# Kernel optimization log

Measured on AMD Instinct MI355X. Metric: run time of the kernel, lower is better.

## Reference

```python
import jax, jax.numpy as jnp
import numpy as np

N = 10000      # nodes
E = 160000     # edges (avg degree 16)
H = 128        # hidden_dim
L = 4          # propagation_depth
G = 64         # graphs in batch
ATOM_V = 119
BOND_V = 5
AVG_D_LOG = 1.0
EPS_SCALE = 1e-8


def setup_inputs() -> dict:
    key = jax.random.key(0)
    ks = jax.random.split(key, 12)
    x = jax.random.randint(ks[0], (N,), 0, ATOM_V)
    edge_index = jax.random.randint(ks[1], (2, E), 0, N)
    edge_attr = jax.random.randint(ks[2], (E,), 0, BOND_V)
    batch = jnp.sort(jax.random.randint(ks[3], (N,), 0, G))
    atom_emb = jax.random.normal(ks[4], (ATOM_V, H), jnp.float32) * 0.1
    bond_emb = jax.random.normal(ks[5], (BOND_V, H), jnp.float32) * 0.1
    pre_W = jax.random.normal(ks[6], (L, 3 * H, H), jnp.float32) / np.sqrt(3 * H)
    pre_b = jnp.zeros((L, H), jnp.float32)
    post_W = jax.random.normal(ks[7], (L, 10 * H, H), jnp.float32) / np.sqrt(10 * H)
    post_b = jnp.zeros((L, H), jnp.float32)
    out_W1 = jax.random.normal(ks[8], (3 * H, H), jnp.float32) / np.sqrt(3 * H)
    out_b1 = jnp.zeros((H,), jnp.float32)
    out_W2 = jax.random.normal(ks[9], (H, 1), jnp.float32) / np.sqrt(H)
    out_b2 = jnp.zeros((1,), jnp.float32)
    return {"x": x, "edge_index": edge_index, "edge_attr": edge_attr, "batch": batch,
            "atom_emb": atom_emb, "bond_emb": bond_emb,
            "pre_W": pre_W, "pre_b": pre_b, "post_W": post_W, "post_b": post_b,
            "out_W1": out_W1, "out_b1": out_b1, "out_W2": out_W2, "out_b2": out_b2}


def _seg_mean_sum_max(v, idx, num_seg, cnt):
    s = jax.ops.segment_sum(v, idx, num_segments=num_seg)
    mean = s / jnp.maximum(cnt, 1.0)[:, None]
    mx = jax.ops.segment_max(v, idx, num_segments=num_seg)
    mx = jnp.where(cnt[:, None] > 0, mx, 0.0)  # empty segments -> 0 (torch scatter)
    return mean, s, mx


def _clean(a):
    return jnp.where(jnp.isnan(a) | jnp.isinf(a), 0.0, a)


def reference(x, edge_index, edge_attr, batch, atom_emb, bond_emb,
              pre_W, pre_b, post_W, post_b, out_W1, out_b1, out_W2, out_b2):
    h = atom_emb[x]            # [N, H] atom encoder
    e = bond_emb[edge_attr]    # [E, H] bond encoder
    row, col = edge_index[0], edge_index[1]
    n = h.shape[0]
    deg = jax.ops.segment_sum(jnp.ones_like(col, jnp.float32), col, num_segments=n)
    D = deg[:, None]
    logD = jnp.log(D + 1.0)
    amp_fac = logD / AVG_D_LOG                       # amplification scaler
    att_fac = AVG_D_LOG / jnp.maximum(logD, EPS_SCALE)  # attenuation scaler
    n_layers = pre_W.shape[0]
    for l in range(n_layers):
        h_in = h
        z2 = jnp.concatenate([h[row], h[col], e], axis=-1)         # [E, 3H]
        msg = z2 @ pre_W[l] + pre_b[l]                             # pretrans (1 layer, no act)
        mean, s, mx = _seg_mean_sum_max(msg, col, n, deg)
        hagg = jnp.concatenate([mean, s, mx], axis=-1)             # [N, 3H]
        hcat = jnp.concatenate([hagg, hagg * amp_fac, hagg * att_fac, h_in], axis=-1)  # [N, 10H]
        h = hcat @ post_W[l] + post_b[l]                           # posttrans (1 layer)
        h = h + h_in                                               # residual
    # readout over graphs
    cnt = jax.ops.segment_sum(jnp.ones((n,), jnp.float32), batch, num_segments=G)
    rmean, rsum, rmax = _seg_mean_sum_max(h, batch, G, cnt)
    r = _clean(jnp.concatenate([rmean, rsum, rmax], axis=-1))      # [G, 3H]
    out = jax.nn.relu(r @ out_W1 + out_b1) @ out_W2 + out_b2       # [G, 1]
    return _clean(out)
```

## Files before the change

kernel.cpp:

```cpp
#include <hip/hip_runtime.h>
#include <hip/hip_bf16.h>
#include <math.h>

#define NN 10000
#define NE 160000
#define HD 128
#define NL 4
#define NG 64

typedef __attribute__((ext_vector_type(8))) short bf16x8;
typedef __attribute__((ext_vector_type(4))) short bf16x4;
typedef __attribute__((ext_vector_type(4))) float f32x4;

static __device__ __forceinline__ short f2bf(float f) {
    unsigned u = __float_as_uint(f);
    unsigned r = (u + 0x7FFFu + ((u >> 16) & 1u)) >> 16;
    return (short)r;
}
static __device__ __forceinline__ float bf2f(short s) {
    return __uint_as_float(((unsigned)(unsigned short)s) << 16);
}

__global__ void setup1_kernel(const int* __restrict__ x, const float* __restrict__ atom_emb,
                              float* __restrict__ h, float* __restrict__ deg,
                              int* __restrict__ cursor) {
    int idx = blockIdx.x * 256 + threadIdx.x;
    if (idx < NN) { deg[idx] = 0.f; cursor[idx] = 0; }
    if (idx < NN * HD) {
        int n = idx >> 7, f = idx & 127;
        h[idx] = atom_emb[x[n] * HD + f];
    }
}

__global__ __launch_bounds__(256) void setup2_kernel(
    const int* __restrict__ col, float* __restrict__ deg,
    const float* __restrict__ bond_emb,
    const float* __restrict__ pre_W, const float* __restrict__ pre_b,
    const float* __restrict__ post_W,
    float* __restrict__ btab, short* __restrict__ pre_Wt, short* __restrict__ post_Wt) {
    int b = blockIdx.x;
    if (b < 625) {
        int e = b * 256 + threadIdx.x;
        if (e < NE) atomicAdd(&deg[col[e]], 1.f);
        return;
    }
    if (b < 645) {
        int lb = b - 625;
        if (threadIdx.x < 128) {
            int l = lb / 5, bb = lb % 5;
            int f = threadIdx.x;
            const float* W2 = pre_W + (size_t)l * 384 * HD + 256 * HD;
            const float* eb = bond_emb + bb * HD;
            float acc = pre_b[l * HD + f];
            for (int k = 0; k < HD; ++k) acc = fmaf(eb[k], W2[k * HD + f], acc);
            btab[(l * 5 + bb) * HD + f] = acc;
        }
        return;
    }
    int idx = (b - 645) * 256 + threadIdx.x;
    if (idx < NL * 4 * 256 * 32) {
        int l = idx >> 15;
        int r = idx & 32767;
        int kblk = r >> 13;
        int rr = r & 8191;
        int j = rr >> 5, k = rr & 31;
        const float* Wl = pre_W + (size_t)l * 384 * HD;
        float v = (j < 128) ? Wl[(kblk * 32 + k) * HD + j]
                            : Wl[(128 + kblk * 32 + k) * HD + (j - 128)];
        pre_Wt[idx] = f2bf(v);
    }
    if (idx < NL * 40 * 128 * 32) {
        int l = idx / 163840;
        int r = idx % 163840;
        int kblk = r >> 12;
        int rr = r & 4095;
        int j = rr >> 5, k = rr & 31;
        post_Wt[idx] = f2bf(post_W[(size_t)l * 163840 + (size_t)(kblk * 32 + k) * HD + j]);
    }
}

__global__ __launch_bounds__(1024) void scan_facs_kernel(const float* __restrict__ deg,
                                                         int* __restrict__ offsets,
                                                         float* __restrict__ amp,
                                                         float* __restrict__ att) {
    __shared__ int s[1024];
    int t = threadIdx.x;
    int base = t * 10;
    int v[10];
    int lsum = 0;
    #pragma unroll
    for (int i = 0; i < 10; ++i) {
        int idx = base + i;
        int d = (idx < NN) ? (int)deg[idx] : 0;
        v[i] = d;
        lsum += d;
        if (idx < NN) {
            float logD = logf((float)d + 1.f);
            amp[idx] = logD;
            att[idx] = 1.f / fmaxf(logD, 1e-8f);
        }
    }
    s[t] = lsum;
    __syncthreads();
    for (int off = 1; off < 1024; off <<= 1) {
        int x2 = (t >= off) ? s[t - off] : 0;
        __syncthreads();
        s[t] += x2;
        __syncthreads();
    }
    int run = s[t] - lsum;
    #pragma unroll
    for (int i = 0; i < 10; ++i) {
        int idx = base + i;
        if (idx < NN) offsets[idx] = run;
        run += v[i];
    }
    if (t == 1023) offsets[NN] = run;
}

__global__ void scatter_kernel(const int* __restrict__ row, const int* __restrict__ col,
                               const int* __restrict__ ea, const int* __restrict__ offsets,
                               int* __restrict__ cursor, int* __restrict__ perm) {
    int e = blockIdx.x * 256 + threadIdx.x;
    if (e < NE) {
        int c = col[e];
        int pos = offsets[c] + atomicAdd(&cursor[c], 1);
        perm[pos] = row[e] | (ea[e] << 14);
    }
}

__global__ __launch_bounds__(256) void pre_gemm_mfma(const float* __restrict__ h,
                                                     const short* __restrict__ Wt,
                                                     short* __restrict__ hw0,
                                                     float* __restrict__ hw1) {
    __shared__ short Ap[16][136];
    int t = threadIdx.x;
    int nb = blockIdx.x * 16;
    {
        int nl = t >> 4, f = (t & 15) * 8;
        int n = nb + nl;
        const float* src = h + (size_t)n * HD + f;
        float4 x0 = *(const float4*)src, x1 = *(const float4*)(src + 4);
        bf16x8 pk;
        pk[0]=f2bf(x0.x); pk[1]=f2bf(x0.y); pk[2]=f2bf(x0.z); pk[3]=f2bf(x0.w);
        pk[4]=f2bf(x1.x); pk[5]=f2bf(x1.y); pk[6]=f2bf(x1.z); pk[7]=f2bf(x1.w);
        *(bf16x8*)&Ap[nl][f] = pk;
    }
    __syncthreads();
    int wave = t >> 6, lane = t & 63;
    int lx = lane & 15, kb = lane >> 4;
    f32x4 acc[4];
    #pragma unroll
    for (int j = 0; j < 4; ++j) acc[j] = (f32x4){0.f, 0.f, 0.f, 0.f};

    for (int ks = 0; ks < 4; ++ks) {
        bf16x8 a = *(const bf16x8*)&Ap[lx][ks * 32 + kb * 8];
        const short* bp = Wt + (size_t)ks * 8192 + (size_t)(wave * 64 + lx) * 32 + kb * 8;
        #pragma unroll
        for (int jj = 0; jj < 4; ++jj) {
            bf16x8 bfr = *(const bf16x8*)(bp + jj * 512);
            acc[jj] = __builtin_amdgcn_mfma_f32_16x16x32_bf16(a, bfr, acc[jj], 0, 0, 0);
        }
    }
    #pragma unroll
    for (int jj = 0; jj < 4; ++jj) {
        int c = wave * 64 + jj * 16 + lx;
        #pragma unroll
        for (int r_ = 0; r_ < 4; ++r_) {
            int n2 = nb + kb * 4 + r_;
            if (c < 128) hw0[(size_t)n2 * HD + c] = f2bf(acc[jj][r_]);
            else         hw1[(size_t)n2 * HD + (c - 128)] = acc[jj][r_];
        }
    }
}

__global__ __launch_bounds__(256) void agg_node_gemm_mfma(
    const short* __restrict__ hw0, const float* __restrict__ hw1,
    const float* __restrict__ btab,
    const int* __restrict__ offsets, const int* __restrict__ perm,
    const float* __restrict__ hin,
    const float* __restrict__ amp, const float* __restrict__ att,
    const short* __restrict__ Wt , const float* __restrict__ bias,
    float* __restrict__ hout,
    const short* __restrict__ nextWt ,
    short* __restrict__ hw0n, float* __restrict__ hw1n) {
    __shared__ short Ap[16][1288];
    __shared__ short Ap2[16][136];
    __shared__ float btab_s[5][128];
    int t = threadIdx.x;
    int nb = blockIdx.x * 16;

    if (t < 160) {
        int b = t >> 5, f4 = (t & 31) * 4;
        *(f32x4*)&btab_s[b][f4] = *(const f32x4*)(btab + b * HD + f4);
    }
    __syncthreads();

    {
        int nl = t >> 4;
        int n = nb + nl;
        int f = (t & 15) * 8;
        int s0 = offsets[n];
        int d = offsets[n + 1] - s0;
        f32x4 sum0 = {0.f,0.f,0.f,0.f}, sum1 = {0.f,0.f,0.f,0.f};
        f32x4 mx0 = {-INFINITY,-INFINITY,-INFINITY,-INFINITY};
        f32x4 mx1 = mx0;
        int i = 0;
        for (; i + 2 <= d; i += 2) {
            int p0 = perm[s0 + i], p1 = perm[s0 + i + 1];
            bf16x8 a0 = *(const bf16x8*)(hw0 + (size_t)(p0 & 16383) * HD + f);
            bf16x8 a1 = *(const bf16x8*)(hw0 + (size_t)(p1 & 16383) * HD + f);
            const float* t0 = &btab_s[p0 >> 14][f];
            const float* t1 = &btab_s[p1 >> 14][f];
            f32x4 b00 = *(const f32x4*)t0, b01 = *(const f32x4*)(t0 + 4);
            f32x4 b10 = *(const f32x4*)t1, b11 = *(const f32x4*)(t1 + 4);
            f32x4 v00, v01, v10, v11;
            #pragma unroll
            for (int q = 0; q < 4; ++q) {
                v00[q] = bf2f(a0[q]) + b00[q];
                v01[q] = bf2f(a0[q + 4]) + b01[q];
                v10[q] = bf2f(a1[q]) + b10[q];
                v11[q] = bf2f(a1[q + 4]) + b11[q];
            }
            sum0 += v00 + v10; sum1 += v01 + v11;
            #pragma unroll
            for (int q = 0; q < 4; ++q) {
                mx0[q] = fmaxf(mx0[q], fmaxf(v00[q], v10[q]));
                mx1[q] = fmaxf(mx1[q], fmaxf(v01[q], v11[q]));
            }
        }
        if (i < d) {
            int p0 = perm[s0 + i];
            bf16x8 a0 = *(const bf16x8*)(hw0 + (size_t)(p0 & 16383) * HD + f);
            const float* t0 = &btab_s[p0 >> 14][f];
            f32x4 b00 = *(const f32x4*)t0, b01 = *(const f32x4*)(t0 + 4);
            f32x4 v00, v01;
            #pragma unroll
            for (int q = 0; q < 4; ++q) {
                v00[q] = bf2f(a0[q]) + b00[q];
                v01[q] = bf2f(a0[q + 4]) + b01[q];
            }
            sum0 += v00; sum1 += v01;
            #pragma unroll
            for (int q = 0; q < 4; ++q) {
                mx0[q] = fmaxf(mx0[q], v00[q]);
                mx1[q] = fmaxf(mx1[q], v01[q]);
            }
        }
        const float* cp = hw1 + (size_t)n * HD + f;
        f32x4 c0 = *(const f32x4*)cp, c1 = *(const f32x4*)(cp + 4);
        f32x4 me0, me1, so0, so1, mo0, mo1;
        if (d > 0) {
            float df = (float)d, di = 1.f / df;
            so0 = sum0 + df * c0;  so1 = sum1 + df * c1;
            me0 = sum0 * di + c0;  me1 = sum1 * di + c1;
            mo0 = mx0 + c0;        mo1 = mx1 + c1;
        } else {
            me0 = (f32x4){0.f,0.f,0.f,0.f}; me1 = me0;
            so0 = me0; so1 = me0; mo0 = me0; mo1 = me0;
        }
        float f_amp = amp[n], f_att = att[n];
        #pragma unroll
        for (int fi = 0; fi < 3; ++fi) {
            float fac = (fi == 0) ? 1.f : ((fi == 1) ? f_amp : f_att);
            #pragma unroll
            for (int ag = 0; ag < 3; ++ag) {
                f32x4 r0 = (ag == 0) ? me0 : ((ag == 1) ? so0 : mo0);
                f32x4 r1 = (ag == 0) ? me1 : ((ag == 1) ? so1 : mo1);
                bf16x8 pk;
                #pragma unroll
                for (int q = 0; q < 4; ++q) {
                    pk[q]     = f2bf(r0[q] * fac);
                    pk[q + 4] = f2bf(r1[q] * fac);
                }
                *(bf16x8*)&Ap[nl][(fi * 3 + ag) * 128 + f] = pk;
            }
        }
        {
            const float* src = hin + (size_t)n * HD + f;
            float4 x0 = *(const float4*)src, x1 = *(const float4*)(src + 4);
            bf16x8 pk;
            pk[0]=f2bf(x0.x); pk[1]=f2bf(x0.y); pk[2]=f2bf(x0.z); pk[3]=f2bf(x0.w);
            pk[4]=f2bf(x1.x); pk[5]=f2bf(x1.y); pk[6]=f2bf(x1.z); pk[7]=f2bf(x1.w);
            *(bf16x8*)&Ap[nl][9 * 128 + f] = pk;
        }
    }
    __syncthreads();

    int wave = t >> 6, lane = t & 63;
    int lx = lane & 15, kb = lane >> 4;
    f32x4 acc0 = {0.f,0.f,0.f,0.f}, acc1 = acc0;
    for (int ks = 0; ks < 40; ++ks) {
        bf16x8 a = *(const bf16x8*)&Ap[lx][ks * 32 + kb * 8];
        const short* bp = Wt + (size_t)ks * 4096 + (size_t)(wave * 32 + lx) * 32 + kb * 8;
        bf16x8 b0 = *(const bf16x8*)bp;
        bf16x8 b1 = *(const bf16x8*)(bp + 512);
        acc0 = __builtin_amdgcn_mfma_f32_16x16x32_bf16(a, b0, acc0, 0, 0, 0);
        acc1 = __builtin_amdgcn_mfma_f32_16x16x32_bf16(a, b1, acc1, 0, 0, 0);
    }
    #pragma unroll
    for (int jj = 0; jj < 2; ++jj) {
        int c = wave * 32 + jj * 16 + lx;
        float bc = bias[c];
        f32x4 av = jj ? acc1 : acc0;
        #pragma unroll
        for (int r_ = 0; r_ < 4; ++r_) {
            int n2 = nb + kb * 4 + r_;
            size_t off = (size_t)n2 * HD + c;
            float ho = av[r_] + bc + hin[off];
            hout[off] = ho;
            Ap2[n2 - nb][c] = f2bf(ho);
        }
    }
    if (nextWt == nullptr) return;
    __syncthreads();

    f32x4 acc[4];
    #pragma unroll
    for (int j = 0; j < 4; ++j) acc[j] = (f32x4){0.f, 0.f, 0.f, 0.f};
    for (int ks = 0; ks < 4; ++ks) {
        bf16x8 a = *(const bf16x8*)&Ap2[lx][ks * 32 + kb * 8];
        const short* bp = nextWt + (size_t)ks * 8192 + (size_t)(wave * 64 + lx) * 32 + kb * 8;
        #pragma unroll
        for (int jj = 0; jj < 4; ++jj) {
            bf16x8 bfr = *(const bf16x8*)(bp + jj * 512);
            acc[jj] = __builtin_amdgcn_mfma_f32_16x16x32_bf16(a, bfr, acc[jj], 0, 0, 0);
        }
    }
    #pragma unroll
    for (int jj = 0; jj < 4; ++jj) {
        int c = wave * 64 + jj * 16 + lx;
        #pragma unroll
        for (int r_ = 0; r_ < 4; ++r_) {
            int n2 = nb + kb * 4 + r_;
            if (c < 128) hw0n[(size_t)n2 * HD + c] = f2bf(acc[jj][r_]);
            else         hw1n[(size_t)n2 * HD + (c - 128)] = acc[jj][r_];
        }
    }
}

__global__ __launch_bounds__(256) void pool_out_kernel(
    const float* __restrict__ h, const int* __restrict__ batch,
    const float* __restrict__ W1, const float* __restrict__ b1,
    const float* __restrict__ W2, const float* __restrict__ b2,
    float* __restrict__ out)
{
    __shared__ float rs[384];
    __shared__ float red[256];
    __shared__ float s2[128], m2[128];
    int g = blockIdx.x, t = threadIdx.x;
    int lo = 0, hi = NN;
    while (lo < hi) { int mid = (lo + hi) >> 1; if (batch[mid] < g) lo = mid + 1; else hi = mid; }
    int lo2 = lo, hi2 = NN;
    while (lo2 < hi2) { int mid = (lo2 + hi2) >> 1; if (batch[mid] < g + 1) lo2 = mid + 1; else hi2 = mid; }
    int cnt = lo2 - lo;
    int f = t & 127, grp = t >> 7;
    float sum = 0.f, mx = -INFINITY;
    for (int n = lo + grp; n < lo2; n += 2) {
        float v = h[(size_t)n * HD + f];
        sum += v; mx = fmaxf(mx, v);
    }
    if (grp == 1) { s2[f] = sum; m2[f] = mx; }
    __syncthreads();
    if (grp == 0) {
        sum += s2[f]; mx = fmaxf(mx, m2[f]);
        float mean = (cnt > 0) ? sum / (float)cnt : 0.f;
        float so = (cnt > 0) ? sum : 0.f;
        float mo = (cnt > 0) ? mx : 0.f;
        if (isnan(mean) || isinf(mean)) mean = 0.f;
        if (isnan(so) || isinf(so)) so = 0.f;
        if (isnan(mo) || isinf(mo)) mo = 0.f;
        rs[f] = mean; rs[128 + f] = so; rs[256 + f] = mo;
    }
    __syncthreads();
    {
        int j = t & 127, kh = t >> 7;
        float acc = 0.f;
        for (int k = kh * 192; k < kh * 192 + 192; ++k)
            acc = fmaf(rs[k], W1[k * HD + j], acc);
        red[t] = acc;
    }
    __syncthreads();
    if (t < 128) {
        float v = fmaxf(red[t] + red[128 + t] + b1[t], 0.f);
        red[t] = v * W2[t];
    }
    __syncthreads();
    for (int s = 64; s > 0; s >>= 1) {
        if (t < s) red[t] += red[t + s];
        __syncthreads();
    }
    if (t == 0) {
        float o = red[0] + b2[0];
        if (isnan(o) || isinf(o)) o = 0.f;
        out[g] = o;
    }
}

extern "C" void kernel_launch(void* const* d_in, const int* in_sizes, int n_in,
                              void* d_out, int out_size, void* d_ws, size_t ws_size,
                              hipStream_t stream)
{
    const int* x          = (const int*)d_in[0];
    const int* ei         = (const int*)d_in[1];
    const int* ea         = (const int*)d_in[2];
    const int* batch      = (const int*)d_in[3];
    const float* atom_emb = (const float*)d_in[4];
    const float* bond_emb = (const float*)d_in[5];
    const float* pre_W    = (const float*)d_in[6];
    const float* pre_b    = (const float*)d_in[7];
    const float* post_W   = (const float*)d_in[8];
    const float* post_b   = (const float*)d_in[9];
    const float* out_W1   = (const float*)d_in[10];
    const float* out_b1   = (const float*)d_in[11];
    const float* out_W2   = (const float*)d_in[12];
    const float* out_b2   = (const float*)d_in[13];
    float* out = (float*)d_out;
    const int* row = ei;
    const int* col = ei + NE;

    char* p = (char*)d_ws;
    auto alloc = [&](size_t bytes) { char* r = p; p += (bytes + 255) & ~(size_t)255; return r; };
    float*    deg     = (float*)alloc((size_t)NN * 4);
    float*    amp     = (float*)alloc((size_t)NN * 4);
    float*    att     = (float*)alloc((size_t)NN * 4);
    int*      offsets = (int*)alloc((size_t)(NN + 1) * 4);
    int*      cursor  = (int*)alloc((size_t)NN * 4);
    int*      perm    = (int*)alloc((size_t)NE * 4);
    float*    hA      = (float*)alloc((size_t)NN * HD * 4);
    float*    hB      = (float*)alloc((size_t)NN * HD * 4);
    short*    hw0A    = (short*)alloc((size_t)NN * HD * 2);
    short*    hw0B    = (short*)alloc((size_t)NN * HD * 2);
    float*    hw1A    = (float*)alloc((size_t)NN * HD * 4);
    float*    hw1B    = (float*)alloc((size_t)NN * HD * 4);
    float*    btab    = (float*)alloc((size_t)NL * 5 * HD * 4);
    short*    pre_Wt  = (short*)alloc((size_t)NL * 4 * 256 * 32 * 2);
    short*    post_Wt = (short*)alloc((size_t)NL * 40 * 128 * 32 * 2);

    setup1_kernel<<<(NN * HD) / 256, 256, 0, stream>>>(x, atom_emb, hA, deg, cursor);
    setup2_kernel<<<645 + (NL * 40 * 128 * 32 + 255) / 256, 256, 0, stream>>>(
        col, deg, bond_emb, pre_W, pre_b, post_W, btab, pre_Wt, post_Wt);
    scan_facs_kernel<<<1, 1024, 0, stream>>>(deg, offsets, amp, att);
    scatter_kernel<<<(NE + 255) / 256, 256, 0, stream>>>(row, col, ea, offsets, cursor, perm);

    pre_gemm_mfma<<<NN / 16, 256, 0, stream>>>(hA, pre_Wt, hw0A, hw1A);

    float* curH = hA;
    float* nxtH = hB;
    for (int l = 0; l < NL; ++l) {
        short* hw0_in  = (l & 1) ? hw0B : hw0A;
        float* hw1_in  = (l & 1) ? hw1B : hw1A;
        short* hw0_out = (l & 1) ? hw0A : hw0B;
        float* hw1_out = (l & 1) ? hw1A : hw1B;
        const short* nextWt = (l + 1 < NL) ? (pre_Wt + (size_t)(l + 1) * 4 * 256 * 32) : nullptr;
        agg_node_gemm_mfma<<<NN / 16, 256, 0, stream>>>(
            hw0_in, hw1_in, btab + (size_t)l * 5 * HD, offsets, perm,
            curH, amp, att, post_Wt + (size_t)l * 40 * 128 * 32,
            post_b + (size_t)l * HD, nxtH, nextWt, hw0_out, hw1_out);
        float* tmp = curH; curH = nxtH; nxtH = tmp;
    }

    pool_out_kernel<<<NG, 256, 0, stream>>>(curH, batch, out_W1, out_b1, out_W2, out_b2, out);
}
```

Baseline: 287.5 us.

## Shrink fused layer LDS by storing only base aggregates and scaling in GEMM

The fused aggregation plus post-transform kernel now keeps only the mean, sum and max aggregates in shared memory, about 19.5 KB instead of roughly 44 KB. The amp and att scaled copies are rebuilt on the fly inside the MFMA loop, and the residual input h is read from global memory and converted per k-step. The edge gather is unrolled to four neighbours per iteration, and launch bounds request 4 blocks per SM. The aim is higher occupancy and more memory-level parallelism in the gather, at the cost of extra bf16 convert and multiply work plus global loads inside the GEMM loop, and an extra bf16 rounding of the scaled terms.

```diff
diff --git a/kernel.cpp b/kernel.cpp
--- a/kernel.cpp
+++ b/kernel.cpp
@@ -7,6 +7,8 @@
 #define HD 128
 #define NL 4
 #define NG 64
+#define NBLK 625
+#define SMEM_BYTES 19584
 
 typedef __attribute__((ext_vector_type(8))) short bf16x8;
 typedef __attribute__((ext_vector_type(4))) short bf16x4;
@@ -129,10 +131,10 @@
     }
 }
 
-__global__ __launch_bounds__(256) void pre_gemm_mfma(const float* __restrict__ h,
-                                                     const short* __restrict__ Wt,
-                                                     short* __restrict__ hw0,
-                                                     float* __restrict__ hw1) {
+__global__ __launch_bounds__(256, 4) void pre_gemm_kernel(const float* __restrict__ h,
+                                                          const short* __restrict__ Wt,
+                                                          short* __restrict__ hw0,
+                                                          float* __restrict__ hw1) {
     __shared__ short Ap[16][136];
     int t = threadIdx.x;
     int nb = blockIdx.x * 16;
@@ -152,7 +154,7 @@
     f32x4 acc[4];
     #pragma unroll
     for (int j = 0; j < 4; ++j) acc[j] = (f32x4){0.f, 0.f, 0.f, 0.f};
-
+    #pragma unroll
     for (int ks = 0; ks < 4; ++ks) {
         bf16x8 a = *(const bf16x8*)&Ap[lx][ks * 32 + kb * 8];
         const short* bp = Wt + (size_t)ks * 8192 + (size_t)(wave * 64 + lx) * 32 + kb * 8;
@@ -174,25 +176,25 @@
     }
 }
 
-__global__ __launch_bounds__(256) void agg_node_gemm_mfma(
-    const short* __restrict__ hw0, const float* __restrict__ hw1,
-    const float* __restrict__ btab,
+__global__ __launch_bounds__(256, 4) void fused_kernel(
+    const short* __restrict__ hw0_in, const float* __restrict__ hw1_in,
+    const float* __restrict__ btabL,
     const int* __restrict__ offsets, const int* __restrict__ perm,
-    const float* __restrict__ hin,
+    const float* __restrict__ curH,
     const float* __restrict__ amp, const float* __restrict__ att,
     const short* __restrict__ Wt , const float* __restrict__ bias,
-    float* __restrict__ hout,
-    const short* __restrict__ nextWt ,
-    short* __restrict__ hw0n, float* __restrict__ hw1n) {
-    __shared__ short Ap[16][1288];
-    __shared__ short Ap2[16][136];
-    __shared__ float btab_s[5][128];
+    float* __restrict__ nxtH,
+    const short* __restrict__ nextWt, short* __restrict__ hw0o, float* __restrict__ hw1o) {
+    __shared__ __align__(16) char smem[SMEM_BYTES];
+    short (*aggB)[3][132] = (short(*)[3][132])smem;
+    float (*btab_s)[128]  = (float(*)[128])(smem + 12672);
+    short (*Ap2)[136]     = (short(*)[136])(smem + 15232);
     int t = threadIdx.x;
     int nb = blockIdx.x * 16;
 
     if (t < 160) {
-        int b = t >> 5, f4 = (t & 31) * 4;
-        *(f32x4*)&btab_s[b][f4] = *(const f32x4*)(btab + b * HD + f4);
+        int bb = t >> 5, f4 = (t & 31) * 4;
+        *(f32x4*)&btab_s[bb][f4] = *(const f32x4*)(btabL + bb * HD + f4);
     }
     __syncthreads();
 
@@ -206,48 +208,47 @@
         f32x4 mx0 = {-INFINITY,-INFINITY,-INFINITY,-INFINITY};
         f32x4 mx1 = mx0;
         int i = 0;
-        for (; i + 2 <= d; i += 2) {
-            int p0 = perm[s0 + i], p1 = perm[s0 + i + 1];
-            bf16x8 a0 = *(const bf16x8*)(hw0 + (size_t)(p0 & 16383) * HD + f);
-            bf16x8 a1 = *(const bf16x8*)(hw0 + (size_t)(p1 & 16383) * HD + f);
+        for (; i + 4 <= d; i += 4) {
+            int p0 = perm[s0 + i],     p1 = perm[s0 + i + 1];
+            int p2 = perm[s0 + i + 2], p3 = perm[s0 + i + 3];
+            bf16x8 a0 = *(const bf16x8*)(hw0_in + (size_t)(p0 & 16383) * HD + f);
+            bf16x8 a1 = *(const bf16x8*)(hw0_in + (size_t)(p1 & 16383) * HD + f);
+            bf16x8 a2 = *(const bf16x8*)(hw0_in + (size_t)(p2 & 16383) * HD + f);
+            bf16x8 a3 = *(const bf16x8*)(hw0_in + (size_t)(p3 & 16383) * HD + f);
             const float* t0 = &btab_s[p0 >> 14][f];
             const float* t1 = &btab_s[p1 >> 14][f];
-            f32x4 b00 = *(const f32x4*)t0, b01 = *(const f32x4*)(t0 + 4);
-            f32x4 b10 = *(const f32x4*)t1, b11 = *(const f32x4*)(t1 + 4);
-            f32x4 v00, v01, v10, v11;
+            const float* t2 = &btab_s[p2 >> 14][f];
+            const float* t3 = &btab_s[p3 >> 14][f];
             #pragma unroll
             for (int q = 0; q < 4; ++q) {
-                v00[q] = bf2f(a0[q]) + b00[q];
-                v01[q] = bf2f(a0[q + 4]) + b01[q];
-                v10[q] = bf2f(a1[q]) + b10[q];
-                v11[q] = bf2f(a1[q + 4]) + b11[q];
+                float v00 = bf2f(a0[q]) + t0[q];
+                float v01 = bf2f(a0[q+4]) + t0[q+4];
+                float v10 = bf2f(a1[q]) + t1[q];
+                float v11 = bf2f(a1[q+4]) + t1[q+4];
+                float v20 = bf2f(a2[q]) + t2[q];
+                float v21 = bf2f(a2[q+4]) + t2[q+4];
+                float v30 = bf2f(a3[q]) + t3[q];
+                float v31 = bf2f(a3[q+4]) + t3[q+4];
+                sum0[q] += (v00 + v10) + (v20 + v30);
+                sum1[q] += (v01 + v11) + (v21 + v31);
+                mx0[q] = fmaxf(fmaxf(fmaxf(mx0[q], v00), fmaxf(v10, v20)), v30);
+                mx1[q] = fmaxf(fmaxf(fmaxf(mx1[q], v01), fmaxf(v11, v21)), v31);
             }
-            sum0 += v00 + v10; sum1 += v01 + v11;
+        }
+        for (; i < d; ++i) {
+            int p0 = perm[s0 + i];
+            bf16x8 a0 = *(const bf16x8*)(hw0_in + (size_t)(p0 & 16383) * HD + f);
+            const float* t0 = &btab_s[p0 >> 14][f];
             #pragma unroll
             for (int q = 0; q < 4; ++q) {
-                mx0[q] = fmaxf(mx0[q], fmaxf(v00[q], v10[q]));
-                mx1[q] = fmaxf(mx1[q], fmaxf(v01[q], v11[q]));
+                float v00 = bf2f(a0[q]) + t0[q];
+                float v01 = bf2f(a0[q+4]) + t0[q+4];
+                sum0[q] += v00; sum1[q] += v01;
+                mx0[q] = fmaxf(mx0[q], v00);
+                mx1[q] = fmaxf(mx1[q], v01);
             }
         }
-        if (i < d) {
-            int p0 = perm[s0 + i];
-            bf16x8 a0 = *(const bf16x8*)(hw0 + (size_t)(p0 & 16383) * HD + f);
-            const float* t0 = &btab_s[p0 >> 14][f];
-            f32x4 b00 = *(const f32x4*)t0, b01 = *(const f32x4*)(t0 + 4);
-            f32x4 v00, v01;
-            #pragma unroll
-            for (int q = 0; q < 4; ++q) {
-                v00[q] = bf2f(a0[q]) + b00[q];
-                v01[q] = bf2f(a0[q + 4]) + b01[q];
-            }
-            sum0 += v00; sum1 += v01;
-            #pragma unroll
-            for (int q = 0; q < 4; ++q) {
-                mx0[q] = fmaxf(mx0[q], v00[q]);
-                mx1[q] = fmaxf(mx1[q], v01[q]);
-            }
-        }
-        const float* cp = hw1 + (size_t)n * HD + f;
+        const float* cp = hw1_in + (size_t)n * HD + f;
         f32x4 c0 = *(const f32x4*)cp, c1 = *(const f32x4*)(cp + 4);
         f32x4 me0, me1, so0, so1, mo0, mo1;
         if (d > 0) {
@@ -259,44 +260,52 @@
             me0 = (f32x4){0.f,0.f,0.f,0.f}; me1 = me0;
             so0 = me0; so1 = me0; mo0 = me0; mo1 = me0;
         }
-        float f_amp = amp[n], f_att = att[n];
-        #pragma unroll
-        for (int fi = 0; fi < 3; ++fi) {
-            float fac = (fi == 0) ? 1.f : ((fi == 1) ? f_amp : f_att);
-            #pragma unroll
-            for (int ag = 0; ag < 3; ++ag) {
-                f32x4 r0 = (ag == 0) ? me0 : ((ag == 1) ? so0 : mo0);
-                f32x4 r1 = (ag == 0) ? me1 : ((ag == 1) ? so1 : mo1);
-                bf16x8 pk;
-                #pragma unroll
-                for (int q = 0; q < 4; ++q) {
-                    pk[q]     = f2bf(r0[q] * fac);
-                    pk[q + 4] = f2bf(r1[q] * fac);
-                }
-                *(bf16x8*)&Ap[nl][(fi * 3 + ag) * 128 + f] = pk;
-            }
-        }
-        {
-            const float* src = hin + (size_t)n * HD + f;
-            float4 x0 = *(const float4*)src, x1 = *(const float4*)(src + 4);
-            bf16x8 pk;
-            pk[0]=f2bf(x0.x); pk[1]=f2bf(x0.y); pk[2]=f2bf(x0.z); pk[3]=f2bf(x0.w);
-            pk[4]=f2bf(x1.x); pk[5]=f2bf(x1.y); pk[6]=f2bf(x1.z); pk[7]=f2bf(x1.w);
-            *(bf16x8*)&Ap[nl][9 * 128 + f] = pk;
-        }
+        bf16x8 pk;
+        #pragma unroll
+        for (int q = 0; q < 4; ++q) { pk[q] = f2bf(me0[q]); pk[q+4] = f2bf(me1[q]); }
+        *(bf16x8*)&aggB[nl][0][f] = pk;
+        #pragma unroll
+        for (int q = 0; q < 4; ++q) { pk[q] = f2bf(so0[q]); pk[q+4] = f2bf(so1[q]); }
+        *(bf16x8*)&aggB[nl][1][f] = pk;
+        #pragma unroll
+        for (int q = 0; q < 4; ++q) { pk[q] = f2bf(mo0[q]); pk[q+4] = f2bf(mo1[q]); }
+        *(bf16x8*)&aggB[nl][2][f] = pk;
     }
     __syncthreads();
 
     int wave = t >> 6, lane = t & 63;
     int lx = lane & 15, kb = lane >> 4;
+    int n_lx = nb + lx;
+    float famp = amp[n_lx], fatt = att[n_lx];
+    const float* hsrc = curH + (size_t)n_lx * HD;
+    const short* bbase = Wt + (size_t)(wave * 32 + lx) * 32 + kb * 8;
     f32x4 acc0 = {0.f,0.f,0.f,0.f}, acc1 = acc0;
+    #pragma unroll
     for (int ks = 0; ks < 40; ++ks) {
-        bf16x8 a = *(const bf16x8*)&Ap[lx][ks * 32 + kb * 8];
-        const short* bp = Wt + (size_t)ks * 4096 + (size_t)(wave * 32 + lx) * 32 + kb * 8;
+        constexpr int KS4096 = 4096;
+        int r = ks >> 2;
+        int kk = (ks & 3) * 32 + kb * 8;
+        bf16x8 afrag;
+        if (r < 9) {
+            int ag = r % 3, fi = r / 3;
+            bf16x8 raw = *(const bf16x8*)&aggB[lx][ag][kk];
+            if (fi == 0) afrag = raw;
+            else {
+                float fac = (fi == 1) ? famp : fatt;
+                #pragma unroll
+                for (int q = 0; q < 8; ++q) afrag[q] = f2bf(bf2f(raw[q]) * fac);
+            }
+        } else {
+            const float* src = hsrc + kk;
+            float4 x0 = *(const float4*)src, x1 = *(const float4*)(src + 4);
+            afrag[0]=f2bf(x0.x); afrag[1]=f2bf(x0.y); afrag[2]=f2bf(x0.z); afrag[3]=f2bf(x0.w);
+            afrag[4]=f2bf(x1.x); afrag[5]=f2bf(x1.y); afrag[6]=f2bf(x1.z); afrag[7]=f2bf(x1.w);
+        }
+        const short* bp = bbase + (size_t)ks * KS4096;
         bf16x8 b0 = *(const bf16x8*)bp;
         bf16x8 b1 = *(const bf16x8*)(bp + 512);
-        acc0 = __builtin_amdgcn_mfma_f32_16x16x32_bf16(a, b0, acc0, 0, 0, 0);
-        acc1 = __builtin_amdgcn_mfma_f32_16x16x32_bf16(a, b1, acc1, 0, 0, 0);
+        acc0 = __builtin_amdgcn_mfma_f32_16x16x32_bf16(afrag, b0, acc0, 0, 0, 0);
+        acc1 = __builtin_amdgcn_mfma_f32_16x16x32_bf16(afrag, b1, acc1, 0, 0, 0);
     }
     #pragma unroll
     for (int jj = 0; jj < 2; ++jj) {
@@ -307,34 +316,35 @@
         for (int r_ = 0; r_ < 4; ++r_) {
             int n2 = nb + kb * 4 + r_;
             size_t off = (size_t)n2 * HD + c;
-            float ho = av[r_] + bc + hin[off];
-            hout[off] = ho;
+            float ho = av[r_] + bc + curH[off];
+            nxtH[off] = ho;
             Ap2[n2 - nb][c] = f2bf(ho);
         }
     }
-    if (nextWt == nullptr) return;
-    __syncthreads();
-
-    f32x4 acc[4];
-    #pragma unroll
-    for (int j = 0; j < 4; ++j) acc[j] = (f32x4){0.f, 0.f, 0.f, 0.f};
-    for (int ks = 0; ks < 4; ++ks) {
-        bf16x8 a = *(const bf16x8*)&Ap2[lx][ks * 32 + kb * 8];
-        const short* bp = nextWt + (size_t)ks * 8192 + (size_t)(wave * 64 + lx) * 32 + kb * 8;
+    if (nextWt != nullptr) {
+        __syncthreads();
+        f32x4 acc[4];
+        #pragma unroll
+        for (int j = 0; j < 4; ++j) acc[j] = (f32x4){0.f, 0.f, 0.f, 0.f};
+        #pragma unroll
+        for (int ks = 0; ks < 4; ++ks) {
+            bf16x8 aa = *(const bf16x8*)&Ap2[lx][ks * 32 + kb * 8];
+            const short* bp = nextWt + (size_t)ks * 8192 + (size_t)(wave * 64 + lx) * 32 + kb * 8;
+            #pragma unroll
+            for (int jj = 0; jj < 4; ++jj) {
+                bf16x8 bfr = *(const bf16x8*)(bp + jj * 512);
+                acc[jj] = __builtin_amdgcn_mfma_f32_16x16x32_bf16(aa, bfr, acc[jj], 0, 0, 0);
+            }
+        }
         #pragma unroll
         for (int jj = 0; jj < 4; ++jj) {
-            bf16x8 bfr = *(const bf16x8*)(bp + jj * 512);
-            acc[jj] = __builtin_amdgcn_mfma_f32_16x16x32_bf16(a, bfr, acc[jj], 0, 0, 0);
-        }
-    }
-    #pragma unroll
-    for (int jj = 0; jj < 4; ++jj) {
-        int c = wave * 64 + jj * 16 + lx;
-        #pragma unroll
-        for (int r_ = 0; r_ < 4; ++r_) {
-            int n2 = nb + kb * 4 + r_;
-            if (c < 128) hw0n[(size_t)n2 * HD + c] = f2bf(acc[jj][r_]);
-            else         hw1n[(size_t)n2 * HD + (c - 128)] = acc[jj][r_];
+            int c = wave * 64 + jj * 16 + lx;
+            #pragma unroll
+            for (int r_ = 0; r_ < 4; ++r_) {
+                int n2 = nb + kb * 4 + r_;
+                if (c < 128) hw0o[(size_t)n2 * HD + c] = f2bf(acc[jj][r_]);
+                else         hw1o[(size_t)n2 * HD + (c - 128)] = acc[jj][r_];
+            }
         }
     }
 }
@@ -442,22 +452,22 @@
         col, deg, bond_emb, pre_W, pre_b, post_W, btab, pre_Wt, post_Wt);
     scan_facs_kernel<<<1, 1024, 0, stream>>>(deg, offsets, amp, att);
     scatter_kernel<<<(NE + 255) / 256, 256, 0, stream>>>(row, col, ea, offsets, cursor, perm);
-
-    pre_gemm_mfma<<<NN / 16, 256, 0, stream>>>(hA, pre_Wt, hw0A, hw1A);
+    pre_gemm_kernel<<<NBLK, 256, 0, stream>>>(hA, pre_Wt, hw0A, hw1A);
 
     float* curH = hA;
     float* nxtH = hB;
+    const short* hw0_in = hw0A;
+    const float* hw1_in = hw1A;
     for (int l = 0; l < NL; ++l) {
-        short* hw0_in  = (l & 1) ? hw0B : hw0A;
-        float* hw1_in  = (l & 1) ? hw1B : hw1A;
         short* hw0_out = (l & 1) ? hw0A : hw0B;
         float* hw1_out = (l & 1) ? hw1A : hw1B;
-        const short* nextWt = (l + 1 < NL) ? (pre_Wt + (size_t)(l + 1) * 4 * 256 * 32) : nullptr;
-        agg_node_gemm_mfma<<<NN / 16, 256, 0, stream>>>(
+        const short* nextWt = (l + 1 < NL) ? (pre_Wt + (size_t)(l + 1) * 32768) : nullptr;
+        fused_kernel<<<NBLK, 256, 0, stream>>>(
             hw0_in, hw1_in, btab + (size_t)l * 5 * HD, offsets, perm,
-            curH, amp, att, post_Wt + (size_t)l * 40 * 128 * 32,
+            curH, amp, att, post_Wt + (size_t)l * 163840,
             post_b + (size_t)l * HD, nxtH, nextWt, hw0_out, hw1_out);
         float* tmp = curH; curH = nxtH; nxtH = tmp;
+        hw0_in = hw0_out; hw1_in = hw1_out;
     }
 
     pool_out_kernel<<<NG, 256, 0, stream>>>(curH, batch, out_W1, out_b1, out_W2, out_b2, out);
```

Measured after the change: 288.6 us. About the same (+0.4%).
